# Kernel optimization log

Measured on AMD Instinct MI355X. Metric: run time of the kernel, lower is better.

The kernel has to match this reference:

```python
import jax, jax.numpy as jnp
import numpy as np

DIM = 256
NEG_SLOPE = 0.01  # torch F.leaky_relu default


def setup_inputs() -> dict:
    key = jax.random.key(0)
    ks = jax.random.split(key, 10)
    B, O, I, D = 16, 64, 512, DIM
    q = jax.random.normal(ks[0], (B, O, D), dtype=jnp.float32)
    k = jax.random.normal(ks[1], (B, I, D), dtype=jnp.float32)
    v = jax.random.normal(ks[2], (B, I, D), dtype=jnp.float32)
    mask = jax.random.randint(ks[3], (B, I), 0, 2).astype(bool)  # 1/True = pad
    s = 1.0 / np.sqrt(2 * D)
    # score MLP: Linear(2D -> D), tanh, Linear(D -> 1)
    W1 = jax.random.normal(ks[4], (D, 2 * D), dtype=jnp.float32) * s
    b1 = jnp.zeros((D,), dtype=jnp.float32)
    W2 = jax.random.normal(ks[5], (1, D), dtype=jnp.float32) * (1.0 / np.sqrt(D))
    b2 = jnp.zeros((1,), dtype=jnp.float32)
    # output projection fw: Linear(D -> D)
    Wf = jax.random.normal(ks[6], (D, D), dtype=jnp.float32) * (1.0 / np.sqrt(D))
    bf = jnp.zeros((D,), dtype=jnp.float32)
    return {"q": q, "k": k, "v": v, "mask": mask,
            "W1": W1, "b1": b1, "W2": W2, "b2": b2, "Wf": Wf, "bf": bf}


def reference(q, k, v, mask, W1, b1, W2, b2, Wf, bf):
    # Linear over concat([q, k]) decomposes exactly: W1 @ [q;k] = W1q@q + W1k@k
    D = q.shape[-1]
    W1q, W1k = W1[:, :D], W1[:, D:]
    qp = jnp.einsum('bod,hd->boh', q, W1q)          # (B, O, D)
    kp = jnp.einsum('bid,hd->bih', k, W1k)          # (B, I, D)
    h = jnp.tanh(qp[:, :, None, :] + kp[:, None, :, :] + b1)  # (B, O, I, D)
    score = jnp.einsum('boih,h->boi', h, W2[0]) + b2[0]       # (B, O, I)
    score = jnp.where(mask[:, None, :], -jnp.inf, score)
    attn = jax.nn.softmax(score, axis=-1)           # (B, O, I)
    out = jnp.einsum('boi,bid->bod', attn, v)       # (B, O, D)
    out = out @ Wf.T + bf                           # dropout in eval mode = identity
    out = jnp.where(out >= 0, out, NEG_SLOPE * out) # leaky_relu
    return out, attn
```

## Files before the change

### kernel.cpp

```cpp
#include <hip/hip_runtime.h>
#include <math.h>

#define DIM 256
#define BATCH 16
#define NO 64
#define NI 512
#define NEG_SLOPE 0.01f
#define CSCALE 2.885390081777927f
#define OT 2

__global__ __launch_bounds__(256, 4) void proj_kernel(
    const float* __restrict__ q, const float* __restrict__ k,
    const float* __restrict__ W1, const float* __restrict__ b1,
    const float* __restrict__ Wf,
    float* __restrict__ Eq, float* __restrict__ Ek2, float* __restrict__ WfT)
{
  __shared__ float smem[8704];

  const int t  = threadIdx.x;
  const int bx = blockIdx.x;

  if (bx >= 576) {
    const int tt = bx - 576;
    const int tr = tt >> 2, tc = tt & 3;
#pragma unroll
    for (int p = 0; p < 4; ++p) {
      int idx = p * 256 + t;
      int row = idx >> 4, j = idx & 15;
      float4 vv = *(const float4*)(Wf + (size_t)(tr * 64 + row) * 256 + tc * 64 + j * 4);
      *(float4*)&smem[row * 68 + j * 4] = vv;
    }
    __syncthreads();
#pragma unroll
    for (int p = 0; p < 4; ++p) {
      int idx = p * 256 + t;
      int row = idx >> 4, j = idx & 15;
      float4 ov;
      ov.x = smem[(j * 4 + 0) * 68 + row];
      ov.y = smem[(j * 4 + 1) * 68 + row];
      ov.z = smem[(j * 4 + 2) * 68 + row];
      ov.w = smem[(j * 4 + 3) * 68 + row];
      *(float4*)(WfT + (size_t)(tc * 64 + row) * 256 + tr * 64 + j * 4) = ov;
    }
    return;
  }

  float* At = smem;
  float* Wt = smem + 4352;

  const int tx = t & 15;
  const int ty = t >> 4;
  const int mt = bx >> 2;
  const int nt = bx & 3;
  const int r0 = mt * 64;
  const int h0 = nt * 64;
  const bool isq = (r0 < BATCH * NO);
  const float* src = isq ? (q + (size_t)r0 * DIM)
                         : (k + (size_t)(r0 - BATCH * NO) * DIM);
  const int coff = isq ? 0 : DIM;

  float acc[4][4] = {};

  for (int c0 = 0; c0 < DIM; c0 += 64) {
    __syncthreads();
#pragma unroll
    for (int p = 0; p < 4; ++p) {
      int idx = p * 256 + t;
      int row = idx >> 4, j = idx & 15;
      float4 av = *(const float4*)(src + (size_t)row * DIM + c0 + j * 4);
      At[(4 * j + 0) * 68 + row] = av.x;
      At[(4 * j + 1) * 68 + row] = av.y;
      At[(4 * j + 2) * 68 + row] = av.z;
      At[(4 * j + 3) * 68 + row] = av.w;
      float4 wv = *(const float4*)(W1 + (size_t)(h0 + row) * (2 * DIM) + coff + c0 + j * 4);
      Wt[(4 * j + 0) * 68 + row] = wv.x;
      Wt[(4 * j + 1) * 68 + row] = wv.y;
      Wt[(4 * j + 2) * 68 + row] = wv.z;
      Wt[(4 * j + 3) * 68 + row] = wv.w;
    }
    __syncthreads();
#pragma unroll
    for (int dk = 0; dk < 64; ++dk) {
      float4 a4 = *(const float4*)&At[dk * 68 + ty * 4];
      float4 w4 = *(const float4*)&Wt[dk * 68 + tx * 4];
      const float ar[4] = {a4.x, a4.y, a4.z, a4.w};
      const float wr[4] = {w4.x, w4.y, w4.z, w4.w};
#pragma unroll
      for (int rr = 0; rr < 4; ++rr)
#pragma unroll
        for (int cc = 0; cc < 4; ++cc)
          acc[rr][cc] = fmaf(ar[rr], wr[cc], acc[rr][cc]);
    }
  }

  if (isq) {
    float4 bv = *(const float4*)(b1 + h0 + tx * 4);
    const float br[4] = {bv.x, bv.y, bv.z, bv.w};
#pragma unroll
    for (int rr = 0; rr < 4; ++rr) {
      int r = r0 + ty * 4 + rr;
      float4 ov;
      ov.x = __builtin_amdgcn_exp2f((acc[rr][0] + br[0]) * CSCALE);
      ov.y = __builtin_amdgcn_exp2f((acc[rr][1] + br[1]) * CSCALE);
      ov.z = __builtin_amdgcn_exp2f((acc[rr][2] + br[2]) * CSCALE);
      ov.w = __builtin_amdgcn_exp2f((acc[rr][3] + br[3]) * CSCALE);
      *(float4*)(Eq + (size_t)r * DIM + h0 + tx * 4) = ov;
    }
  } else {
    int ig0 = r0 - BATCH * NO;
    int b  = ig0 >> 9;
    int i0 = (ig0 & 511) + ty * 4;
    int h2b = (h0 + tx * 4) >> 1;
#pragma unroll
    for (int c2 = 0; c2 < 2; ++c2) {
      size_t base = ((size_t)(b * 128 + h2b + c2) * NI + i0) * 2;
      float4 w0, w1;
      w0.x = __builtin_amdgcn_exp2f(acc[0][2 * c2]     * CSCALE);
      w0.y = __builtin_amdgcn_exp2f(acc[0][2 * c2 + 1] * CSCALE);
      w0.z = __builtin_amdgcn_exp2f(acc[1][2 * c2]     * CSCALE);
      w0.w = __builtin_amdgcn_exp2f(acc[1][2 * c2 + 1] * CSCALE);
      w1.x = __builtin_amdgcn_exp2f(acc[2][2 * c2]     * CSCALE);
      w1.y = __builtin_amdgcn_exp2f(acc[2][2 * c2 + 1] * CSCALE);
      w1.z = __builtin_amdgcn_exp2f(acc[3][2 * c2]     * CSCALE);
      w1.w = __builtin_amdgcn_exp2f(acc[3][2 * c2 + 1] * CSCALE);
      *(float4*)(Ek2 + base)     = w0;
      *(float4*)(Ek2 + base + 4) = w1;
    }
  }
}

__device__ __forceinline__ void f4arr(float4 v, float* a) {
  a[0] = v.x; a[1] = v.y; a[2] = v.z; a[3] = v.w;
}

__global__ __launch_bounds__(512, 4) void attn_kernel(
    const float* __restrict__ Eq, const float* __restrict__ Ek2,
    const float* __restrict__ v, const int* __restrict__ mask,
    const float* __restrict__ W2, const float* __restrict__ b2,
    const float* __restrict__ WfT, const float* __restrict__ bf,
    float* __restrict__ out, float* __restrict__ attn_out)
{
  __shared__ float sc[OT][NI];
  __shared__ float pvp[8][OT][DIM];
  __shared__ float o0[OT][DIM];
  __shared__ float red4[8][OT];
  __shared__ float redw[8];

  const int t    = threadIdx.x;
  const int lane = t & 63;
  const int wid  = t >> 6;

  const int blk  = blockIdx.x;
  const int tile = (blk & 7) * 64 + (blk >> 3);
  const int b    = tile >> 5;
  const int bo0  = b * 64 + (tile & 31) * OT;

  float partial = (t < DIM) ? W2[t] : 0.f;
#pragma unroll
  for (int off = 32; off >= 1; off >>= 1) partial += __shfl_xor(partial, off, 64);
  if (lane == 0) redw[wid] = partial;
  __syncthreads();
  float sumw2 = 0.f;
#pragma unroll
  for (int w = 0; w < 8; ++w) sumw2 += redw[w];
  const float base = sumw2 + b2[0];

  const int i = t;
  const float2* kb = (const float2*)Ek2 + (size_t)b * 128 * NI;
  const float* qrow0 = Eq + (size_t)(bo0 + 0) * DIM;
  const float* qrow1 = Eq + (size_t)(bo0 + 1) * DIM;

  float acc0 = 0.f, acc1 = 0.f;
#pragma unroll 4
  for (int h4 = 0; h4 < 64; ++h4) {
    float wr[4], q0[4], q1[4];
    f4arr(*(const float4*)(W2 + h4 * 4), wr);
    f4arr(*(const float4*)(qrow0 + h4 * 4), q0);
    f4arr(*(const float4*)(qrow1 + h4 * 4), q1);
    float2 kva = kb[(size_t)(h4 * 2 + 0) * NI + i];
    float2 kvb = kb[(size_t)(h4 * 2 + 1) * NI + i];
    const float kv[4] = {kva.x, kva.y, kvb.x, kvb.y};
#pragma unroll
    for (int e = 0; e < 4; ++e) {
      float d0 = fmaf(q0[e], kv[e], 1.f);
      acc0 = fmaf(wr[e], __builtin_amdgcn_rcpf(d0), acc0);
      float d1 = fmaf(q1[e], kv[e], 1.f);
      acc1 = fmaf(wr[e], __builtin_amdgcn_rcpf(d1), acc1);
    }
  }

  const int mv = mask[(size_t)b * NI + i];
  float s0 = base - 2.f * acc0;
  float s1 = base - 2.f * acc1;
  if (mv) { s0 = -INFINITY; s1 = -INFINITY; }

  float m0 = s0, m1 = s1;
#pragma unroll
  for (int off = 32; off >= 1; off >>= 1) {
    m0 = fmaxf(m0, __shfl_xor(m0, off, 64));
    m1 = fmaxf(m1, __shfl_xor(m1, off, 64));
  }
  __syncthreads();
  if (lane == 0) { red4[wid][0] = m0; red4[wid][1] = m1; }
  __syncthreads();
  m0 = red4[0][0]; m1 = red4[0][1];
#pragma unroll
  for (int w = 1; w < 8; ++w) {
    m0 = fmaxf(m0, red4[w][0]);
    m1 = fmaxf(m1, red4[w][1]);
  }

  float p0 = __builtin_amdgcn_exp2f((s0 - m0) * 1.4426950408889634f);
  float p1 = __builtin_amdgcn_exp2f((s1 - m1) * 1.4426950408889634f);
  float ps0 = p0, ps1 = p1;
#pragma unroll
  for (int off = 32; off >= 1; off >>= 1) {
    ps0 += __shfl_xor(ps0, off, 64);
    ps1 += __shfl_xor(ps1, off, 64);
  }
  __syncthreads();
  if (lane == 0) { red4[wid][0] = ps0; red4[wid][1] = ps1; }
  __syncthreads();
  float ss0 = 0.f, ss1 = 0.f;
#pragma unroll
  for (int w = 0; w < 8; ++w) { ss0 += red4[w][0]; ss1 += red4[w][1]; }
  const float a0 = p0 * __builtin_amdgcn_rcpf(ss0);
  const float a1 = p1 * __builtin_amdgcn_rcpf(ss1);
  sc[0][i] = a0;
  sc[1][i] = a1;
  attn_out[(size_t)(bo0 + 0) * NI + i] = a0;
  attn_out[(size_t)(bo0 + 1) * NI + i] = a1;
  __syncthreads();

  {
    const int d4 = lane;
    float4 av0 = {0.f, 0.f, 0.f, 0.f};
    float4 av1 = {0.f, 0.f, 0.f, 0.f};
    const float4* vb4 = (const float4*)(v + (size_t)b * NI * DIM);
    for (int ib = wid * 64; ib < wid * 64 + 64; ib += 4) {
      float sa0[4], sa1[4];
      f4arr(*(const float4*)&sc[0][ib], sa0);
      f4arr(*(const float4*)&sc[1][ib], sa1);
#pragma unroll
      for (int j = 0; j < 4; ++j) {
        float4 vv = vb4[(size_t)(ib + j) * 64 + d4];
        av0.x = fmaf(sa0[j], vv.x, av0.x);
        av0.y = fmaf(sa0[j], vv.y, av0.y);
        av0.z = fmaf(sa0[j], vv.z, av0.z);
        av0.w = fmaf(sa0[j], vv.w, av0.w);
        av1.x = fmaf(sa1[j], vv.x, av1.x);
        av1.y = fmaf(sa1[j], vv.y, av1.y);
        av1.z = fmaf(sa1[j], vv.z, av1.z);
        av1.w = fmaf(sa1[j], vv.w, av1.w);
      }
    }
    *(float4*)&pvp[wid][0][d4 * 4] = av0;
    *(float4*)&pvp[wid][1][d4 * 4] = av1;
  }
  __syncthreads();
  {
    int oo = t >> 8, d = t & 255;
    float sacc = 0.f;
#pragma unroll
    for (int w = 0; w < 8; ++w) sacc += pvp[w][oo][d];
    o0[oo][d] = sacc;
  }
  __syncthreads();

  {
    const int oo = t >> 8;
    const int d  = t & 255;
    float f = 0.f;
#pragma unroll 8
    for (int e4 = 0; e4 < 64; ++e4) {
      float oa[4];
      f4arr(*(const float4*)&o0[oo][e4 * 4], oa);
#pragma unroll
      for (int c = 0; c < 4; ++c)
        f = fmaf(oa[c], WfT[(size_t)(e4 * 4 + c) * DIM + d], f);
    }
    f += bf[d];
    f = (f >= 0.f) ? f : NEG_SLOPE * f;
    out[(size_t)(bo0 + oo) * DIM + d] = f;
  }
}

extern "C" void kernel_launch(void* const* d_in, const int* in_sizes, int n_in,
                              void* d_out, int out_size, void* d_ws, size_t ws_size,
                              hipStream_t stream) {
  const float* q    = (const float*)d_in[0];
  const float* k    = (const float*)d_in[1];
  const float* v    = (const float*)d_in[2];
  const int*   mask = (const int*)d_in[3];
  const float* W1   = (const float*)d_in[4];
  const float* b1   = (const float*)d_in[5];
  const float* W2   = (const float*)d_in[6];
  const float* b2   = (const float*)d_in[7];
  const float* Wf   = (const float*)d_in[8];
  const float* bf   = (const float*)d_in[9];

  float* out      = (float*)d_out;
  float* attn_out = out + (size_t)BATCH * NO * DIM;

  float* Eq  = (float*)d_ws;
  float* Ek2 = Eq + (size_t)BATCH * NO * DIM;
  float* WfT = Ek2 + (size_t)BATCH * DIM * NI;

  proj_kernel<<<592, 256, 0, stream>>>(q, k, W1, b1, Wf, Eq, Ek2, WfT);
  attn_kernel<<<(BATCH * NO) / OT, 512, 0, stream>>>(Eq, Ek2, v, mask, W2, b2,
                                                     WfT, bf, out, attn_out);
}
```

Baseline: 149.4 us.

## Store Ek transposed and stage it through LDS with register prefetch

The projection kernel now writes exp(k-projection) in a plain [b][h][i] layout instead of the interleaved float2 layout. The attention kernel loads 8 h-rows at a time as float4 into registers, stores them to a shared buffer, and prefetches the next chunk while computing from LDS. This is meant to hide global load latency in the score loop and use wider coalesced loads. In exchange it adds 16KB of LDS and two barriers per chunk, which may lower occupancy.

```diff
diff --git a/kernel.cpp b/kernel.cpp
--- a/kernel.cpp
+++ b/kernel.cpp
@@ -13,7 +13,7 @@
     const float* __restrict__ q, const float* __restrict__ k,
     const float* __restrict__ W1, const float* __restrict__ b1,
     const float* __restrict__ Wf,
-    float* __restrict__ Eq, float* __restrict__ Ek2, float* __restrict__ WfT)
+    float* __restrict__ Eq, float* __restrict__ EkT, float* __restrict__ WfT)
 {
   __shared__ float smem[8704];
 
@@ -110,21 +110,15 @@
     int ig0 = r0 - BATCH * NO;
     int b  = ig0 >> 9;
     int i0 = (ig0 & 511) + ty * 4;
-    int h2b = (h0 + tx * 4) >> 1;
-#pragma unroll
-    for (int c2 = 0; c2 < 2; ++c2) {
-      size_t base = ((size_t)(b * 128 + h2b + c2) * NI + i0) * 2;
-      float4 w0, w1;
-      w0.x = __builtin_amdgcn_exp2f(acc[0][2 * c2]     * CSCALE);
-      w0.y = __builtin_amdgcn_exp2f(acc[0][2 * c2 + 1] * CSCALE);
-      w0.z = __builtin_amdgcn_exp2f(acc[1][2 * c2]     * CSCALE);
-      w0.w = __builtin_amdgcn_exp2f(acc[1][2 * c2 + 1] * CSCALE);
-      w1.x = __builtin_amdgcn_exp2f(acc[2][2 * c2]     * CSCALE);
-      w1.y = __builtin_amdgcn_exp2f(acc[2][2 * c2 + 1] * CSCALE);
-      w1.z = __builtin_amdgcn_exp2f(acc[3][2 * c2]     * CSCALE);
-      w1.w = __builtin_amdgcn_exp2f(acc[3][2 * c2 + 1] * CSCALE);
-      *(float4*)(Ek2 + base)     = w0;
-      *(float4*)(Ek2 + base + 4) = w1;
+#pragma unroll
+    for (int cc = 0; cc < 4; ++cc) {
+      int h = h0 + tx * 4 + cc;
+      float4 ov;
+      ov.x = __builtin_amdgcn_exp2f(acc[0][cc] * CSCALE);
+      ov.y = __builtin_amdgcn_exp2f(acc[1][cc] * CSCALE);
+      ov.z = __builtin_amdgcn_exp2f(acc[2][cc] * CSCALE);
+      ov.w = __builtin_amdgcn_exp2f(acc[3][cc] * CSCALE);
+      *(float4*)(EkT + ((size_t)(b * 256 + h)) * NI + i0) = ov;
     }
   }
 }
@@ -134,12 +128,13 @@
 }
 
 __global__ __launch_bounds__(512, 4) void attn_kernel(
-    const float* __restrict__ Eq, const float* __restrict__ Ek2,
+    const float* __restrict__ Eq, const float* __restrict__ EkT,
     const float* __restrict__ v, const int* __restrict__ mask,
     const float* __restrict__ W2, const float* __restrict__ b2,
     const float* __restrict__ WfT, const float* __restrict__ bf,
     float* __restrict__ out, float* __restrict__ attn_out)
 {
+  __shared__ float EkS[8 * NI];
   __shared__ float sc[OT][NI];
   __shared__ float pvp[8][OT][DIM];
   __shared__ float o0[OT][DIM];
@@ -166,26 +161,38 @@
   const float base = sumw2 + b2[0];
 
   const int i = t;
-  const float2* kb = (const float2*)Ek2 + (size_t)b * 128 * NI;
+  const float* kb = EkT + (size_t)b * DIM * NI;
   const float* qrow0 = Eq + (size_t)(bo0 + 0) * DIM;
   const float* qrow1 = Eq + (size_t)(bo0 + 1) * DIM;
 
+  float4 r0 = ((const float4*)kb)[t];
+  float4 r1 = ((const float4*)kb)[t + 512];
+
   float acc0 = 0.f, acc1 = 0.f;
-#pragma unroll 4
-  for (int h4 = 0; h4 < 64; ++h4) {
-    float wr[4], q0[4], q1[4];
-    f4arr(*(const float4*)(W2 + h4 * 4), wr);
-    f4arr(*(const float4*)(qrow0 + h4 * 4), q0);
-    f4arr(*(const float4*)(qrow1 + h4 * 4), q1);
-    float2 kva = kb[(size_t)(h4 * 2 + 0) * NI + i];
-    float2 kvb = kb[(size_t)(h4 * 2 + 1) * NI + i];
-    const float kv[4] = {kva.x, kva.y, kvb.x, kvb.y};
-#pragma unroll
-    for (int e = 0; e < 4; ++e) {
-      float d0 = fmaf(q0[e], kv[e], 1.f);
-      acc0 = fmaf(wr[e], __builtin_amdgcn_rcpf(d0), acc0);
-      float d1 = fmaf(q1[e], kv[e], 1.f);
-      acc1 = fmaf(wr[e], __builtin_amdgcn_rcpf(d1), acc1);
+  for (int c = 0; c < 32; ++c) {
+    __syncthreads();
+    ((float4*)EkS)[t]       = r0;
+    ((float4*)EkS)[t + 512] = r1;
+    __syncthreads();
+    if (c + 1 < 32) {
+      const float4* s4 = (const float4*)(kb + (size_t)(c + 1) * 8 * NI);
+      r0 = s4[t];
+      r1 = s4[t + 512];
+    }
+    float wr[8], q0r[8], q1r[8];
+    f4arr(*(const float4*)(W2 + c * 8), wr);
+    f4arr(*(const float4*)(W2 + c * 8 + 4), wr + 4);
+    f4arr(*(const float4*)(qrow0 + c * 8), q0r);
+    f4arr(*(const float4*)(qrow0 + c * 8 + 4), q0r + 4);
+    f4arr(*(const float4*)(qrow1 + c * 8), q1r);
+    f4arr(*(const float4*)(qrow1 + c * 8 + 4), q1r + 4);
+#pragma unroll
+    for (int hh = 0; hh < 8; ++hh) {
+      float kv = EkS[hh * NI + i];
+      float d0 = fmaf(q0r[hh], kv, 1.f);
+      acc0 = fmaf(wr[hh], __builtin_amdgcn_rcpf(d0), acc0);
+      float d1 = fmaf(q1r[hh], kv, 1.f);
+      acc1 = fmaf(wr[hh], __builtin_amdgcn_rcpf(d1), acc1);
     }
   }
 
@@ -303,10 +310,10 @@
   float* attn_out = out + (size_t)BATCH * NO * DIM;
 
   float* Eq  = (float*)d_ws;
-  float* Ek2 = Eq + (size_t)BATCH * NO * DIM;
-  float* WfT = Ek2 + (size_t)BATCH * DIM * NI;
-
-  proj_kernel<<<592, 256, 0, stream>>>(q, k, W1, b1, Wf, Eq, Ek2, WfT);
-  attn_kernel<<<(BATCH * NO) / OT, 512, 0, stream>>>(Eq, Ek2, v, mask, W2, b2,
+  float* EkT = Eq + (size_t)BATCH * NO * DIM;
+  float* WfT = EkT + (size_t)BATCH * DIM * NI;
+
+  proj_kernel<<<592, 256, 0, stream>>>(q, k, W1, b1, Wf, Eq, EkT, WfT);
+  attn_kernel<<<(BATCH * NO) / OT, 512, 0, stream>>>(Eq, EkT, v, mask, W2, b2,
                                                      WfT, bf, out, attn_out);
 }
```

New measurement: 154.7 us. +3.6%, slower.
